# Kernel tuning notes

Hardware: AMD Instinct MI355X
Metric: run time of the kernel (lower is better)

The kernel has to match this reference:

```python
import jax, jax.numpy as jnp
import numpy as np

C = 256  # channels (depthwise: groups == out_channels == in_channels)


def _dwconv(x, w, b):
    # x: [B,C,H,W], w: [C,1,3,3] (OIHW), b: [C]; depthwise 3x3, padding=1
    out = jax.lax.conv_general_dilated(
        x, w,
        window_strides=(1, 1),
        padding=((1, 1), (1, 1)),
        dimension_numbers=('NCHW', 'OIHW', 'NCHW'),
        feature_group_count=C,
    )
    return out + b[None, :, None, None]


def setup_inputs() -> dict:
    key = jax.random.key(0)
    k1, k2, k3, k4 = jax.random.split(key, 4)
    B, H, W = 8, 128, 128
    x = jax.random.normal(k1, (B, C, H, W), dtype=jnp.float32)
    y = jax.random.normal(k2, (B, C, H, W), dtype=jnp.float32)
    # torch Conv2d default init: U(-sqrt(k), sqrt(k)), k = 1/(fan_in) = 1/(1*3*3)
    bound = 1.0 / np.sqrt(9.0)
    conv_w = jax.random.uniform(k3, (C, 1, 3, 3), dtype=jnp.float32, minval=-bound, maxval=bound)
    conv_b = jax.random.uniform(k4, (C,), dtype=jnp.float32, minval=-bound, maxval=bound)
    return {"x": x, "y": y, "conv_w": conv_w, "conv_b": conv_b}


def reference(x, y, conv_w, conv_b):
    # Forget gate
    f_feat = _dwconv(y, conv_w, conv_b)
    f_gate = jax.nn.sigmoid(f_feat)
    # Update gate
    u_gate = f_gate * jnp.tanh(f_feat)
    # Stage and output (same conv weights applied again)
    x_stage = x * f_gate + u_gate
    output_y = jnp.tanh(_dwconv(x_stage, conv_w, conv_b)) * f_gate + y + y
    return output_y
```

## Files before the change

### kernel.cpp

```cpp
#include <hip/hip_runtime.h>
#include <math.h>

#define HW   128
#define BH   8
#define C_CH 256

struct R12 { float l0, l1; float4 a, b; float r0, r1; };
struct R10 { float l;      float4 a, b; float r;      };

__device__ __forceinline__ void sig_tanh(float s, float& fg, float& th) {
    float sc = fminf(15.f, fmaxf(-15.f, s));
    float t  = __expf(-sc);
    float t2 = t * t;
    fg = __builtin_amdgcn_rcpf(1.f + t);
    th = fmaf(2.f, __builtin_amdgcn_rcpf(1.f + t2), -1.f);
}

__device__ __forceinline__ float tanh_fast(float s) {
    float sc = fminf(15.f, fmaxf(-15.f, s));
    float t2 = __expf(-2.f * sc);
    return fmaf(2.f, __builtin_amdgcn_rcpf(1.f + t2), -1.f);
}

__device__ __forceinline__ void facc(float w0, float w1, float w2,
                                     const R12& y, R10& s) {
    s.l   = fmaf(w0, y.l0,  fmaf(w1, y.l1,  fmaf(w2, y.a.x, s.l)));
    s.a.x = fmaf(w0, y.l1,  fmaf(w1, y.a.x, fmaf(w2, y.a.y, s.a.x)));
    s.a.y = fmaf(w0, y.a.x, fmaf(w1, y.a.y, fmaf(w2, y.a.z, s.a.y)));
    s.a.z = fmaf(w0, y.a.y, fmaf(w1, y.a.z, fmaf(w2, y.a.w, s.a.z)));
    s.a.w = fmaf(w0, y.a.z, fmaf(w1, y.a.w, fmaf(w2, y.b.x, s.a.w)));
    s.b.x = fmaf(w0, y.a.w, fmaf(w1, y.b.x, fmaf(w2, y.b.y, s.b.x)));
    s.b.y = fmaf(w0, y.b.x, fmaf(w1, y.b.y, fmaf(w2, y.b.z, s.b.y)));
    s.b.z = fmaf(w0, y.b.y, fmaf(w1, y.b.z, fmaf(w2, y.b.w, s.b.z)));
    s.b.w = fmaf(w0, y.b.z, fmaf(w1, y.b.w, fmaf(w2, y.r0,  s.b.w)));
    s.r   = fmaf(w0, y.b.w, fmaf(w1, y.r0,  fmaf(w2, y.r1,  s.r)));
}

__device__ __forceinline__ void oacc(float w0, float w1, float w2,
                                     const R10& v, float4& s0, float4& s1) {
    s0.x = fmaf(w0, v.l,   fmaf(w1, v.a.x, fmaf(w2, v.a.y, s0.x)));
    s0.y = fmaf(w0, v.a.x, fmaf(w1, v.a.y, fmaf(w2, v.a.z, s0.y)));
    s0.z = fmaf(w0, v.a.y, fmaf(w1, v.a.z, fmaf(w2, v.a.w, s0.z)));
    s0.w = fmaf(w0, v.a.z, fmaf(w1, v.a.w, fmaf(w2, v.b.x, s0.w)));
    s1.x = fmaf(w0, v.a.w, fmaf(w1, v.b.x, fmaf(w2, v.b.y, s1.x)));
    s1.y = fmaf(w0, v.b.x, fmaf(w1, v.b.y, fmaf(w2, v.b.z, s1.y)));
    s1.z = fmaf(w0, v.b.y, fmaf(w1, v.b.z, fmaf(w2, v.b.w, s1.z)));
    s1.w = fmaf(w0, v.b.z, fmaf(w1, v.b.w, fmaf(w2, v.r,   s1.w)));
}

__global__ __launch_bounds__(256, 4) void fused_gated_dwconv_nh(
    const float* __restrict__ x, const float* __restrict__ y,
    const float* __restrict__ w, const float* __restrict__ b,
    float* __restrict__ out)
{
    const int tid   = threadIdx.x;
    const int s     = tid & 15;
    const int band  = tid >> 4;
    const int plane = blockIdx.x;
    const int c     = plane & (C_CH - 1);
    const int rb    = band * BH;
    const int col0  = s * 8;
    const bool sL = (s == 0), sR = (s == 15);

    const size_t poff = (size_t)plane * (HW * HW);
    const float* yp = y + poff;
    const float* xp = x + poff;
    float*       op = out + poff;

    float wk[9];
    #pragma unroll
    for (int k = 0; k < 9; ++k) wk[k] = w[c * 9 + k];
    const float bias = b[c];

    R12 yw[3];
    R10 xw[3];
    float4 fga[2], fgb[2];

    #pragma unroll
    for (int t = 0; t < BH + 4; ++t) {
        {
            int gy = rb - 2 + t;
            bool iny = (unsigned)gy < (unsigned)HW;
            const float* p = yp + (size_t)(iny ? gy : 0) * HW;
            float2 lv = *reinterpret_cast<const float2*>(p + (sL ? col0 : col0 - 2));
            float4 av = *reinterpret_cast<const float4*>(p + col0);
            float4 bv = *reinterpret_cast<const float4*>(p + col0 + 4);
            float2 rv = *reinterpret_cast<const float2*>(p + (sR ? col0 : col0 + 8));
            R12 Y;
            bool okL = iny && !sL, okR = iny && !sR;
            Y.l0 = okL ? lv.x : 0.f;
            Y.l1 = okL ? lv.y : 0.f;
            Y.a  = iny ? av : make_float4(0.f, 0.f, 0.f, 0.f);
            Y.b  = iny ? bv : make_float4(0.f, 0.f, 0.f, 0.f);
            Y.r0 = okR ? rv.x : 0.f;
            Y.r1 = okR ? rv.y : 0.f;
            yw[t % 3] = Y;
        }
        if (t >= 2) {
            int q = rb - 3 + t;
            bool inx = (unsigned)q < (unsigned)HW;
            const float* p = xp + (size_t)(inx ? q : 0) * HW;
            float  xl = *(p + (sL ? col0 : col0 - 1));
            float4 xa = *reinterpret_cast<const float4*>(p + col0);
            float4 xb = *reinterpret_cast<const float4*>(p + col0 + 4);
            float  xr = *(p + (sR ? col0 : col0 + 8));

            R10 F;
            F.l = bias; F.a = make_float4(bias, bias, bias, bias); F.b = F.a; F.r = bias;
            facc(wk[0], wk[1], wk[2], yw[(t - 2) % 3], F);
            facc(wk[3], wk[4], wk[5], yw[(t - 1) % 3], F);
            facc(wk[6], wk[7], wk[8], yw[t % 3],       F);

            float fgl, thl, fgr, thr;
            float4 fa, ta, fb, tb;
            sig_tanh(F.l,   fgl,  thl);
            sig_tanh(F.a.x, fa.x, ta.x);
            sig_tanh(F.a.y, fa.y, ta.y);
            sig_tanh(F.a.z, fa.z, ta.z);
            sig_tanh(F.a.w, fa.w, ta.w);
            sig_tanh(F.b.x, fb.x, tb.x);
            sig_tanh(F.b.y, fb.y, tb.y);
            sig_tanh(F.b.z, fb.z, tb.z);
            sig_tanh(F.b.w, fb.w, tb.w);
            sig_tanh(F.r,   fgr,  thr);

            R10 XS;
            XS.l   = (inx && !sL) ? fgl * (xl + thl) : 0.f;
            XS.a.x = fa.x * (xa.x + ta.x);
            XS.a.y = fa.y * (xa.y + ta.y);
            XS.a.z = fa.z * (xa.z + ta.z);
            XS.a.w = fa.w * (xa.w + ta.w);
            XS.b.x = fb.x * (xb.x + tb.x);
            XS.b.y = fb.y * (xb.y + tb.y);
            XS.b.z = fb.z * (xb.z + tb.z);
            XS.b.w = fb.w * (xb.w + tb.w);
            XS.r   = (inx && !sR) ? fgr * (xr + thr) : 0.f;
            if (!inx) {
                XS.a = make_float4(0.f, 0.f, 0.f, 0.f);
                XS.b = make_float4(0.f, 0.f, 0.f, 0.f);
            }
            xw[t % 3] = XS;
            fga[t & 1] = fa; fgb[t & 1] = fb;
        }
        if (t >= 4) {
            int r = rb - 4 + t;
            float4 s0 = make_float4(bias, bias, bias, bias), s1 = s0;
            oacc(wk[0], wk[1], wk[2], xw[(t - 2) % 3], s0, s1);
            oacc(wk[3], wk[4], wk[5], xw[(t - 1) % 3], s0, s1);
            oacc(wk[6], wk[7], wk[8], xw[t % 3],       s0, s1);

            const float4 fa = fga[(t + 1) & 1];
            const float4 fb = fgb[(t + 1) & 1];
            const R12&  Y  = yw[(t - 2) % 3];

            float4 o0, o1;
            o0.x = fmaf(tanh_fast(s0.x), fa.x, 2.f * Y.a.x);
            o0.y = fmaf(tanh_fast(s0.y), fa.y, 2.f * Y.a.y);
            o0.z = fmaf(tanh_fast(s0.z), fa.z, 2.f * Y.a.z);
            o0.w = fmaf(tanh_fast(s0.w), fa.w, 2.f * Y.a.w);
            o1.x = fmaf(tanh_fast(s1.x), fb.x, 2.f * Y.b.x);
            o1.y = fmaf(tanh_fast(s1.y), fb.y, 2.f * Y.b.y);
            o1.z = fmaf(tanh_fast(s1.z), fb.z, 2.f * Y.b.z);
            o1.w = fmaf(tanh_fast(s1.w), fb.w, 2.f * Y.b.w);

            float* po = op + (size_t)r * HW + col0;
            *reinterpret_cast<float4*>(po)     = o0;
            *reinterpret_cast<float4*>(po + 4) = o1;
        }
    }
}

extern "C" void kernel_launch(void* const* d_in, const int* in_sizes, int n_in,
                              void* d_out, int out_size, void* d_ws, size_t ws_size,
                              hipStream_t stream) {
    const float* x = (const float*)d_in[0];
    const float* y = (const float*)d_in[1];
    const float* w = (const float*)d_in[2];
    const float* b = (const float*)d_in[3];
    float* out = (float*)d_out;

    const int planes = in_sizes[0] / (HW * HW);
    dim3 grid(planes);
    dim3 block(256);
    fused_gated_dwconv_nh<<<grid, block, 0, stream>>>(x, y, w, b, out);
}
```

Measured before the change: 100.0 us.

## Cut register pressure: fp16-packed gate buffer, scalar weights, shared reciprocal

```diff
diff --git a/kernel.cpp b/kernel.cpp
--- a/kernel.cpp
+++ b/kernel.cpp
@@ -5,19 +5,28 @@
 #define BH   8
 #define C_CH 256
 
+typedef __fp16 h2 __attribute__((ext_vector_type(2)));
+
 struct R12 { float l0, l1; float4 a, b; float r0, r1; };
 struct R10 { float l;      float4 a, b; float r;      };
 
+__device__ __forceinline__ float uload(float v) {
+    return __int_as_float(__builtin_amdgcn_readfirstlane(__float_as_int(v)));
+}
+
 __device__ __forceinline__ void sig_tanh(float s, float& fg, float& th) {
-    float sc = fminf(15.f, fmaxf(-15.f, s));
+    float sc = fminf(20.f, fmaxf(-20.f, s));
     float t  = __expf(-sc);
     float t2 = t * t;
-    fg = __builtin_amdgcn_rcpf(1.f + t);
-    th = fmaf(2.f, __builtin_amdgcn_rcpf(1.f + t2), -1.f);
+    float a  = 1.f + t;
+    float b2 = 1.f + t2;
+    float D  = __builtin_amdgcn_rcpf(a * b2);
+    fg = b2 * D;
+    th = fmaf(2.f * a, D, -1.f);
 }
 
 __device__ __forceinline__ float tanh_fast(float s) {
-    float sc = fminf(15.f, fmaxf(-15.f, s));
+    float sc = fminf(20.f, fmaxf(-20.f, s));
     float t2 = __expf(-2.f * sc);
     return fmaf(2.f, __builtin_amdgcn_rcpf(1.f + t2), -1.f);
 }
@@ -48,7 +57,7 @@
     s1.w = fmaf(w0, v.b.z, fmaf(w1, v.b.w, fmaf(w2, v.r,   s1.w)));
 }
 
-__global__ __launch_bounds__(256, 4) void fused_gated_dwconv_nh(
+__global__ __launch_bounds__(256, 5) void fused_gated_dwconv_s(
     const float* __restrict__ x, const float* __restrict__ y,
     const float* __restrict__ w, const float* __restrict__ b,
     float* __restrict__ out)
@@ -69,12 +78,15 @@
 
     float wk[9];
     #pragma unroll
-    for (int k = 0; k < 9; ++k) wk[k] = w[c * 9 + k];
-    const float bias = b[c];
+    for (int k = 0; k < 9; ++k) wk[k] = uload(w[c * 9 + k]);
+    const float bias = uload(b[c]);
 
     R12 yw[3];
     R10 xw[3];
-    float4 fga[2], fgb[2];
+    h2 fgp0a, fgp0b, fgp0c, fgp0d;
+    h2 fgp1a, fgp1b, fgp1c, fgp1d;
+
+    const float4 z4 = make_float4(0.f, 0.f, 0.f, 0.f);
 
     #pragma unroll
     for (int t = 0; t < BH + 4; ++t) {
@@ -90,8 +102,8 @@
             bool okL = iny && !sL, okR = iny && !sR;
             Y.l0 = okL ? lv.x : 0.f;
             Y.l1 = okL ? lv.y : 0.f;
-            Y.a  = iny ? av : make_float4(0.f, 0.f, 0.f, 0.f);
-            Y.b  = iny ? bv : make_float4(0.f, 0.f, 0.f, 0.f);
+            Y.a  = iny ? av : z4;
+            Y.b  = iny ? bv : z4;
             Y.r0 = okR ? rv.x : 0.f;
             Y.r1 = okR ? rv.y : 0.f;
             yw[t % 3] = Y;
@@ -135,12 +147,20 @@
             XS.b.z = fb.z * (xb.z + tb.z);
             XS.b.w = fb.w * (xb.w + tb.w);
             XS.r   = (inx && !sR) ? fgr * (xr + thr) : 0.f;
-            if (!inx) {
-                XS.a = make_float4(0.f, 0.f, 0.f, 0.f);
-                XS.b = make_float4(0.f, 0.f, 0.f, 0.f);
+            if (!inx) { XS.a = z4; XS.b = z4; }
+            xw[t % 3] = XS;
+
+            if (t & 1) {
+                fgp1a = __builtin_amdgcn_cvt_pkrtz(fa.x, fa.y);
+                fgp1b = __builtin_amdgcn_cvt_pkrtz(fa.z, fa.w);
+                fgp1c = __builtin_amdgcn_cvt_pkrtz(fb.x, fb.y);
+                fgp1d = __builtin_amdgcn_cvt_pkrtz(fb.z, fb.w);
+            } else {
+                fgp0a = __builtin_amdgcn_cvt_pkrtz(fa.x, fa.y);
+                fgp0b = __builtin_amdgcn_cvt_pkrtz(fa.z, fa.w);
+                fgp0c = __builtin_amdgcn_cvt_pkrtz(fb.x, fb.y);
+                fgp0d = __builtin_amdgcn_cvt_pkrtz(fb.z, fb.w);
             }
-            xw[t % 3] = XS;
-            fga[t & 1] = fa; fgb[t & 1] = fb;
         }
         if (t >= 4) {
             int r = rb - 4 + t;
@@ -149,19 +169,21 @@
             oacc(wk[3], wk[4], wk[5], xw[(t - 1) % 3], s0, s1);
             oacc(wk[6], wk[7], wk[8], xw[t % 3],       s0, s1);
 
-            const float4 fa = fga[(t + 1) & 1];
-            const float4 fb = fgb[(t + 1) & 1];
-            const R12&  Y  = yw[(t - 2) % 3];
+            h2 Pa, Pb, Pc, Pd;
+            if ((t - 1) & 1) { Pa = fgp1a; Pb = fgp1b; Pc = fgp1c; Pd = fgp1d; }
+            else             { Pa = fgp0a; Pb = fgp0b; Pc = fgp0c; Pd = fgp0d; }
+
+            const R12& Y = yw[(t - 2) % 3];
 
             float4 o0, o1;
-            o0.x = fmaf(tanh_fast(s0.x), fa.x, 2.f * Y.a.x);
-            o0.y = fmaf(tanh_fast(s0.y), fa.y, 2.f * Y.a.y);
-            o0.z = fmaf(tanh_fast(s0.z), fa.z, 2.f * Y.a.z);
-            o0.w = fmaf(tanh_fast(s0.w), fa.w, 2.f * Y.a.w);
-            o1.x = fmaf(tanh_fast(s1.x), fb.x, 2.f * Y.b.x);
-            o1.y = fmaf(tanh_fast(s1.y), fb.y, 2.f * Y.b.y);
-            o1.z = fmaf(tanh_fast(s1.z), fb.z, 2.f * Y.b.z);
-            o1.w = fmaf(tanh_fast(s1.w), fb.w, 2.f * Y.b.w);
+            o0.x = fmaf(tanh_fast(s0.x), (float)Pa[0], 2.f * Y.a.x);
+            o0.y = fmaf(tanh_fast(s0.y), (float)Pa[1], 2.f * Y.a.y);
+            o0.z = fmaf(tanh_fast(s0.z), (float)Pb[0], 2.f * Y.a.z);
+            o0.w = fmaf(tanh_fast(s0.w), (float)Pb[1], 2.f * Y.a.w);
+            o1.x = fmaf(tanh_fast(s1.x), (float)Pc[0], 2.f * Y.b.x);
+            o1.y = fmaf(tanh_fast(s1.y), (float)Pc[1], 2.f * Y.b.y);
+            o1.z = fmaf(tanh_fast(s1.z), (float)Pd[0], 2.f * Y.b.z);
+            o1.w = fmaf(tanh_fast(s1.w), (float)Pd[1], 2.f * Y.b.w);
 
             float* po = op + (size_t)r * HW + col0;
             *reinterpret_cast<float4*>(po)     = o0;
@@ -182,5 +204,5 @@
     const int planes = in_sizes[0] / (HW * HW);
     dim3 grid(planes);
     dim3 block(256);
-    fused_gated_dwconv_nh<<<grid, block, 0, stream>>>(x, y, w, b, out);
-}
+    fused_gated_dwconv_s<<<grid, block, 0, stream>>>(x, y, w, b, out);
+}
```

After: 206.4 us. +106.3%, slower.
